# Kernel tuning notes

Measured on AMD Instinct MI355X. Metric: run time of the kernel, lower is better.

## Reference

```python
import jax, jax.numpy as jnp
import numpy as np

B, S, D, H = 2, 2048, 1024, 16
DH = D // H
EPS = 1e-12


def setup_inputs() -> dict:
    key = jax.random.key(0)
    ks = jax.random.split(key, 8)
    return {
        "query": jax.random.normal(ks[0], (B, S, D), jnp.float32),
        "key": jax.random.normal(ks[1], (B, S, D), jnp.float32),
        "value": jax.random.normal(ks[2], (B, S, D), jnp.float32),
        "mask": jax.random.randint(ks[3], (B, S), 0, 2, jnp.int32),
        "Wq": jax.random.normal(ks[4], (D, D), jnp.float32) * 0.02,
        "bq": jnp.zeros((D,), jnp.float32),
        "Wk": jax.random.normal(ks[5], (D, D), jnp.float32) * 0.02,
        "bk": jnp.zeros((D,), jnp.float32),
        "Wv": jax.random.normal(ks[6], (D, D), jnp.float32) * 0.02,
        "bv": jnp.zeros((D,), jnp.float32),
        "gamma": jnp.ones((D,), jnp.float32),
        "beta": jnp.zeros((D,), jnp.float32),
    }


def _split_heads(x):
    # [B,S,D] -> [B,H,S,DH]
    return x.reshape(B, S, H, DH).transpose(0, 2, 1, 3)


def reference(query, key, value, mask, Wq, bq, Wk, bk, Wv, bv, gamma, beta):
    q = _split_heads(query @ Wq + bq)
    k = _split_heads(key @ Wk + bk)
    v = _split_heads(value @ Wv + bv)

    scale = 1.0 / jnp.sqrt(jnp.float32(DH))
    scores = jnp.einsum("bhqd,bhkd->bhqk", q, k) * scale  # [B,H,S,S]
    maskf = mask.astype(jnp.float32)  # [B,S]
    scores = scores - 10000.0 * (1.0 - maskf[:, None, None, :])
    attn = jax.nn.softmax(scores, axis=-1)  # dropout disabled (eval mode)

    h = jnp.einsum("bhqk,bhkd->bhqd", attn, v)
    h = h.transpose(0, 2, 1, 3).reshape(B, S, D)

    x = query + h
    u = jnp.mean(x, axis=-1, keepdims=True)
    s = jnp.mean((x - u) ** 2, axis=-1, keepdims=True)
    xn = (x - u) / jnp.sqrt(s + EPS)
    return gamma * xn + beta
```

## Files before the change

kernel.cpp:

```cpp
#include <hip/hip_runtime.h>
#include <math.h>

#define B_  2
#define S_  2048
#define D_  1024
#define H_  16
#define DH_ 64
#define M_  (B_*S_)

typedef short v8s __attribute__((ext_vector_type(8)));
typedef float v4f __attribute__((ext_vector_type(4)));
typedef unsigned short u16;

__device__ __forceinline__ u16 f2bf(float f) {
    unsigned u = __float_as_uint(f);
    u = u + 0x7FFFu + ((u >> 16) & 1u);
    return (u16)(u >> 16);
}

__global__ __launch_bounds__(256)
void cvt_bf16_kernel(const float* __restrict__ X0, const float* __restrict__ X1,
                     const float* __restrict__ X2, u16* __restrict__ Y)
{
    const float* X = (blockIdx.y == 0) ? X0 : (blockIdx.y == 1) ? X1 : X2;
    u16* out = Y + (size_t)blockIdx.y * M_ * D_;
    const size_t i = ((size_t)blockIdx.x * 256 + threadIdx.x) * 8;
    float4 a = *(const float4*)&X[i];
    float4 b = *(const float4*)&X[i + 4];
    u16 tmp[8];
    tmp[0] = f2bf(a.x); tmp[1] = f2bf(a.y); tmp[2] = f2bf(a.z); tmp[3] = f2bf(a.w);
    tmp[4] = f2bf(b.x); tmp[5] = f2bf(b.y); tmp[6] = f2bf(b.z); tmp[7] = f2bf(b.w);
    *(v8s*)&out[i] = *(v8s*)&tmp[0];
}

__global__ __launch_bounds__(256)
void transpose_w_kernel(const float* __restrict__ W0, const float* __restrict__ W1,
                        const float* __restrict__ W2, u16* __restrict__ WtAll)
{
    __shared__ u16 TS[64][66];
    const float* W = (blockIdx.z == 0) ? W0 : (blockIdx.z == 1) ? W1 : W2;
    u16* out = WtAll + (size_t)blockIdx.z * D_ * D_;
    const int k0 = blockIdx.x * 64;
    const int n0 = blockIdx.y * 64;
    const int t = threadIdx.x;
    const int r = t >> 2, c = t & 3;

    #pragma unroll
    for (int u = 0; u < 4; ++u) {
        int nc = (c + 4 * u) * 4;
        float4 v = *(const float4*)&W[(size_t)(k0 + r) * D_ + n0 + nc];
        TS[r][nc + 0] = f2bf(v.x); TS[r][nc + 1] = f2bf(v.y);
        TS[r][nc + 2] = f2bf(v.z); TS[r][nc + 3] = f2bf(v.w);
    }
    __syncthreads();
    u16 tmp[16];
    #pragma unroll
    for (int u = 0; u < 16; ++u) tmp[u] = TS[c * 16 + u][r];
    u16* dst = &out[(size_t)(n0 + r) * D_ + k0 + c * 16];
    *(v8s*)&dst[0] = *(v8s*)&tmp[0];
    *(v8s*)&dst[8] = *(v8s*)&tmp[8];
}

__global__ __launch_bounds__(256)
void qkv_gemm_kernel(const u16* __restrict__ XbfAll, const u16* __restrict__ WtAll,
                     const float* __restrict__ bq, const float* __restrict__ bk2,
                     const float* __restrict__ bv2,
                     u16* __restrict__ Qh, u16* __restrict__ Kh, u16* __restrict__ Vh)
{
    __shared__ u16 SA[128 * 32];
    __shared__ u16 SB[128 * 32];

    const int z = blockIdx.z;
    const u16* X  = XbfAll + (size_t)z * M_ * D_;
    const u16* Wt = WtAll  + (size_t)z * D_ * D_;
    const float* bias = (z == 0) ? bq : (z == 1) ? bk2 : bv2;
    u16* Y = (z == 0) ? Qh : (z == 1) ? Kh : Vh;

    const int t = threadIdx.x;
    const int lane = t & 63;
    const int w = t >> 6;
    const int g = lane >> 4;
    const int l15 = lane & 15;
    const int wr = (w >> 1) * 64;
    const int wc = (w & 1) * 64;
    const int row0 = blockIdx.y * 128;
    const int col0 = blockIdx.x * 128;

    v4f acc[4][4];
    #pragma unroll
    for (int m = 0; m < 4; ++m)
        #pragma unroll
        for (int n = 0; n < 4; ++n)
            acc[m][n] = (v4f){0.f, 0.f, 0.f, 0.f};

    const int r0s = w * 32 + (lane >> 2);
    const int cphys = lane & 3;

    for (int k0 = 0; k0 < D_; k0 += 32) {
        __syncthreads();
        #pragma unroll
        for (int c = 0; c < 2; ++c) {
            const int r = r0s + c * 16;
            const int clog = cphys ^ ((r >> 1) & 3);
            const u16* asrc = &X [(size_t)(row0 + r) * D_ + k0 + clog * 8];
            const u16* bsrc = &Wt[(size_t)(col0 + r) * D_ + k0 + clog * 8];
            __builtin_amdgcn_global_load_lds(
                (const __attribute__((address_space(1))) void*)asrc,
                (__attribute__((address_space(3))) void*)&SA[(w * 32 + c * 16) * 32],
                16, 0, 0);
            __builtin_amdgcn_global_load_lds(
                (const __attribute__((address_space(1))) void*)bsrc,
                (__attribute__((address_space(3))) void*)&SB[(w * 32 + c * 16) * 32],
                16, 0, 0);
        }
        __syncthreads();

        v8s av[4], bvv[4];
        #pragma unroll
        for (int m = 0; m < 4; ++m) {
            const int r = wr + m * 16 + l15;
            av[m] = *(const v8s*)&SA[r * 32 + (g ^ ((r >> 1) & 3)) * 8];
        }
        #pragma unroll
        for (int n = 0; n < 4; ++n) {
            const int r = wc + n * 16 + l15;
            bvv[n] = *(const v8s*)&SB[r * 32 + (g ^ ((r >> 1) & 3)) * 8];
        }
        #pragma unroll
        for (int m = 0; m < 4; ++m)
            #pragma unroll
            for (int n = 0; n < 4; ++n)
                acc[m][n] = __builtin_amdgcn_mfma_f32_16x16x32_bf16(av[m], bvv[n], acc[m][n], 0, 0, 0);
    }

    #pragma unroll
    for (int n = 0; n < 4; ++n) {
        int col = col0 + wc + n * 16 + l15;
        float bb = bias[col];
        int h = col >> 6, d = col & 63;
        #pragma unroll
        for (int m = 0; m < 4; ++m) {
            #pragma unroll
            for (int i = 0; i < 4; ++i) {
                int row = row0 + wr + m * 16 + g * 4 + i;
                int b = row >> 11, s = row & (S_ - 1);
                Y[(((size_t)(b * H_ + h)) * S_ + s) * DH_ + d] = f2bf(acc[m][n][i] + bb);
            }
        }
    }
}

__global__ __launch_bounds__(256)
void transpose_v_kernel(const u16* __restrict__ Vh, u16* __restrict__ Vt)
{
    __shared__ u16 TS[64][66];
    const int bh = blockIdx.y;
    const int s0 = blockIdx.x * 64;
    const int t = threadIdx.x;
    const int r = t >> 2, c = t & 3;

    {
        const u16* src = Vh + ((size_t)(bh * S_ + s0 + r)) * DH_ + c * 16;
        v8s a = *(const v8s*)&src[0];
        v8s b = *(const v8s*)&src[8];
        *(v8s*)&TS[r][c * 16]     = a;
        *(v8s*)&TS[r][c * 16 + 8] = b;
    }
    __syncthreads();
    u16 tmp[16];
    #pragma unroll
    for (int u = 0; u < 16; ++u) tmp[u] = TS[c * 16 + u][r];
    u16* dst = Vt + ((size_t)(bh * DH_ + r)) * S_ + s0 + c * 16;
    *(v8s*)&dst[0] = *(v8s*)&tmp[0];
    *(v8s*)&dst[8] = *(v8s*)&tmp[8];
}

__global__ __launch_bounds__(256)
void attn_kernel(const u16* __restrict__ Qh, const u16* __restrict__ Kh,
                 const u16* __restrict__ Vt, const int* __restrict__ mask,
                 float* __restrict__ Hout)
{
    __shared__ u16 Ks[64][64];
    __shared__ u16 Vs[64][64];
    __shared__ u16 Ps[4][16][64];
    __shared__ float mb[64];

    const int t = threadIdx.x;
    const int lane = t & 63;
    const int w = t >> 6;
    const int g = lane >> 4;
    const int l15 = lane & 15;
    const int bh = blockIdx.y;
    const int b = bh >> 4;
    const int h = bh & 15;
    const int q0 = blockIdx.x * 64;

    const float SC = 0.18033688011112042f;
    const float MBIAS = -14426.950408889634f;

    v8s aq[2];
    {
        const u16* qb = Qh + ((size_t)bh * S_ + q0 + w * 16 + l15) * DH_;
        aq[0] = *(const v8s*)&qb[g * 8];
        aq[1] = *(const v8s*)&qb[32 + g * 8];
    }

    float lsum[4] = {0.f, 0.f, 0.f, 0.f};
    v4f Of[4];
    #pragma unroll
    for (int j = 0; j < 4; ++j) Of[j] = (v4f){0.f, 0.f, 0.f, 0.f};

    const int sk = t >> 3;
    const int sj = t & 7;
    const int swz_s = (sj ^ (sk & 7)) * 8;

    for (int kt = 0; kt < S_ / 64; ++kt) {
        const int kbase = kt * 64;
        const u16* ksrc0 = Kh + ((size_t)bh * S_ + kbase + sk) * DH_ + sj * 8;
        const u16* ksrc1 = Kh + ((size_t)bh * S_ + kbase + sk + 32) * DH_ + sj * 8;
        v8s kr0 = *(const v8s*)ksrc0;
        v8s kr1 = *(const v8s*)ksrc1;
        const u16* vsrc0 = Vt + ((size_t)bh * DH_ + sk) * S_ + kbase + sj * 8;
        const u16* vsrc1 = Vt + ((size_t)bh * DH_ + sk + 32) * S_ + kbase + sj * 8;
        v8s vr0 = *(const v8s*)vsrc0;
        v8s vr1 = *(const v8s*)vsrc1;
        int mv = 0;
        if (t < 64) mv = mask[b * S_ + kbase + t];

        __syncthreads();
        *(v8s*)&Ks[sk][swz_s]      = kr0;
        *(v8s*)&Ks[sk + 32][swz_s] = kr1;
        *(v8s*)&Vs[sk][swz_s]      = vr0;
        *(v8s*)&Vs[sk + 32][swz_s] = vr1;
        if (t < 64) mb[t] = mv ? 0.0f : MBIAS;
        __syncthreads();

        v4f sc4[4];
        #pragma unroll
        for (int j = 0; j < 4; ++j) sc4[j] = (v4f){0.f, 0.f, 0.f, 0.f};
        #pragma unroll
        for (int j = 0; j < 4; ++j) {
            const int kcol = j * 16 + l15;
            const int sx = kcol & 7;
            v8s bk0 = *(const v8s*)&Ks[kcol][((0 * 4 + g) ^ sx) * 8];
            v8s bk1 = *(const v8s*)&Ks[kcol][((1 * 4 + g) ^ sx) * 8];
            sc4[j] = __builtin_amdgcn_mfma_f32_16x16x32_bf16(aq[0], bk0, sc4[j], 0, 0, 0);
            sc4[j] = __builtin_amdgcn_mfma_f32_16x16x32_bf16(aq[1], bk1, sc4[j], 0, 0, 0);
        }
        float mbj[4];
        #pragma unroll
        for (int j = 0; j < 4; ++j) mbj[j] = mb[j * 16 + l15];

        #pragma unroll
        for (int i = 0; i < 4; ++i) {
            float p0 = __builtin_amdgcn_exp2f(fmaf(sc4[0][i], SC, mbj[0]));
            float p1 = __builtin_amdgcn_exp2f(fmaf(sc4[1][i], SC, mbj[1]));
            float p2 = __builtin_amdgcn_exp2f(fmaf(sc4[2][i], SC, mbj[2]));
            float p3 = __builtin_amdgcn_exp2f(fmaf(sc4[3][i], SC, mbj[3]));
            lsum[i] += (p0 + p1) + (p2 + p3);
            const int q = g * 4 + i;
            const int swz = 8 * (q & 7);
            Ps[w][q][(0 * 16 + l15) ^ swz] = f2bf(p0);
            Ps[w][q][(1 * 16 + l15) ^ swz] = f2bf(p1);
            Ps[w][q][(2 * 16 + l15) ^ swz] = f2bf(p2);
            Ps[w][q][(3 * 16 + l15) ^ swz] = f2bf(p3);
        }

        const int sq = l15 & 7;
        v8s pa0 = *(const v8s*)&Ps[w][l15][((0 + g) ^ sq) * 8];
        v8s pa1 = *(const v8s*)&Ps[w][l15][((4 + g) ^ sq) * 8];
        #pragma unroll
        for (int j = 0; j < 4; ++j) {
            const int dcol = j * 16 + l15;
            const int sx = dcol & 7;
            v8s bv0 = *(const v8s*)&Vs[dcol][((0 + g) ^ sx) * 8];
            v8s bv1 = *(const v8s*)&Vs[dcol][((4 + g) ^ sx) * 8];
            Of[j] = __builtin_amdgcn_mfma_f32_16x16x32_bf16(pa0, bv0, Of[j], 0, 0, 0);
            Of[j] = __builtin_amdgcn_mfma_f32_16x16x32_bf16(pa1, bv1, Of[j], 0, 0, 0);
        }
    }

    #pragma unroll
    for (int i = 0; i < 4; ++i) {
        lsum[i] += __shfl_xor(lsum[i], 1, 64);
        lsum[i] += __shfl_xor(lsum[i], 2, 64);
        lsum[i] += __shfl_xor(lsum[i], 4, 64);
        lsum[i] += __shfl_xor(lsum[i], 8, 64);
    }
    float inv[4];
    #pragma unroll
    for (int i = 0; i < 4; ++i) inv[i] = 1.0f / lsum[i];
    #pragma unroll
    for (int j = 0; j < 4; ++j) {
        #pragma unroll
        for (int i = 0; i < 4; ++i) {
            int q = q0 + w * 16 + g * 4 + i;
            Hout[((size_t)(b * S_ + q)) * D_ + h * DH_ + j * 16 + l15] = Of[j][i] * inv[i];
        }
    }
}

__global__ __launch_bounds__(256)
void ln_kernel(const float* __restrict__ query, const float* __restrict__ Hout,
               const float* __restrict__ gamma, const float* __restrict__ beta,
               float* __restrict__ out)
{
    __shared__ float ws1[4], ws2[4];
    const int row = blockIdx.x;
    const int tid = threadIdx.x;
    const size_t base = (size_t)row * D_ + tid * 4;

    float4 xq = *(const float4*)&query[base];
    float4 xh = *(const float4*)&Hout[base];
    float x[4] = { xq.x + xh.x, xq.y + xh.y, xq.z + xh.z, xq.w + xh.w };

    float sum = x[0] + x[1] + x[2] + x[3];
    float sq  = x[0]*x[0] + x[1]*x[1] + x[2]*x[2] + x[3]*x[3];
    #pragma unroll
    for (int off = 32; off >= 1; off >>= 1) {
        sum += __shfl_down(sum, off, 64);
        sq  += __shfl_down(sq,  off, 64);
    }
    if ((tid & 63) == 0) { ws1[tid >> 6] = sum; ws2[tid >> 6] = sq; }
    __syncthreads();
    sum = ws1[0] + ws1[1] + ws1[2] + ws1[3];
    sq  = ws2[0] + ws2[1] + ws2[2] + ws2[3];

    const float u    = sum * (1.0f / D_);
    const float var  = sq * (1.0f / D_) - u * u;
    const float rstd = rsqrtf(var + 1e-12f);

    float4 gv = *(const float4*)&gamma[tid * 4];
    float4 bv = *(const float4*)&beta[tid * 4];
    float4 o;
    o.x = gv.x * (x[0] - u) * rstd + bv.x;
    o.y = gv.y * (x[1] - u) * rstd + bv.y;
    o.z = gv.z * (x[2] - u) * rstd + bv.z;
    o.w = gv.w * (x[3] - u) * rstd + bv.w;
    *(float4*)&out[base] = o;
}

extern "C" void kernel_launch(void* const* d_in, const int* in_sizes, int n_in,
                              void* d_out, int out_size, void* d_ws, size_t ws_size,
                              hipStream_t stream)
{
    const float* query = (const float*)d_in[0];
    const float* key   = (const float*)d_in[1];
    const float* value = (const float*)d_in[2];
    const int*   mask  = (const int*)d_in[3];
    const float* Wq    = (const float*)d_in[4];
    const float* bq    = (const float*)d_in[5];
    const float* Wk    = (const float*)d_in[6];
    const float* bk    = (const float*)d_in[7];
    const float* Wv    = (const float*)d_in[8];
    const float* bv    = (const float*)d_in[9];
    const float* gamma = (const float*)d_in[10];
    const float* beta  = (const float*)d_in[11];
    float* out = (float*)d_out;

    char* ws = (char*)d_ws;
    u16* Xbf = (u16*)ws;                      ws += (size_t)3 * M_ * D_ * sizeof(u16);
    u16* Wt  = (u16*)ws;                      ws += (size_t)3 * D_ * D_ * sizeof(u16);
    u16* Qh  = (u16*)ws;                      ws += (size_t)M_ * D_ * sizeof(u16);
    u16* Kh  = (u16*)ws;                      ws += (size_t)M_ * D_ * sizeof(u16);
    u16* Vh  = (u16*)ws;                      ws += (size_t)M_ * D_ * sizeof(u16);
    u16* Vt  = (u16*)ws;                      ws += (size_t)M_ * D_ * sizeof(u16);
    float* Ho = (float*)ws;

    cvt_bf16_kernel<<<dim3(M_ * D_ / 2048, 3), 256, 0, stream>>>(query, key, value, Xbf);
    transpose_w_kernel<<<dim3(16, 16, 3), 256, 0, stream>>>(Wq, Wk, Wv, Wt);
    qkv_gemm_kernel<<<dim3(D_ / 128, M_ / 128, 3), 256, 0, stream>>>(
        Xbf, Wt, bq, bk, bv, Qh, Kh, Vh);
    transpose_v_kernel<<<dim3(S_ / 64, B_ * H_), 256, 0, stream>>>(Vh, Vt);
    attn_kernel<<<dim3(S_ / 64, B_ * H_), 256, 0, stream>>>(Qh, Kh, Vt, mask, Ho);
    ln_kernel<<<M_, 256, 0, stream>>>(query, Ho, gamma, beta, out);
}
```

Measured before the change: 238.3 us.

## Use 32x32 MFMA with BK=64 in QKV GEMM, fuse V transpose into epilogue

Rewrites the QKV projection GEMM to use 32x32x16 bf16 MFMA tiles with a 64-wide K step and an XOR-swizzled LDS layout, halving the number of K-loop barriers. The V output is written directly in transposed layout from the GEMM epilogue, which removes the separate transpose kernel and its round trip through memory. The attention P conversion switches from round-to-nearest to truncating bf16, saving a few ALU ops per element at a small accuracy cost. The transposed V stores are strided by sequence, so they may coalesce poorly.

```diff
diff --git a/kernel.cpp b/kernel.cpp
--- a/kernel.cpp
+++ b/kernel.cpp
@@ -8,14 +8,18 @@
 #define DH_ 64
 #define M_  (B_*S_)
 
-typedef short v8s __attribute__((ext_vector_type(8)));
-typedef float v4f __attribute__((ext_vector_type(4)));
+typedef short v8s  __attribute__((ext_vector_type(8)));
+typedef float v4f  __attribute__((ext_vector_type(4)));
+typedef float f32x16 __attribute__((ext_vector_type(16)));
 typedef unsigned short u16;
 
 __device__ __forceinline__ u16 f2bf(float f) {
     unsigned u = __float_as_uint(f);
     u = u + 0x7FFFu + ((u >> 16) & 1u);
     return (u16)(u >> 16);
+}
+__device__ __forceinline__ u16 f2bf_t(float f) {
+    return (u16)(__float_as_uint(f) >> 16);
 }
 
 __global__ __launch_bounds__(256)
@@ -65,114 +69,100 @@
 void qkv_gemm_kernel(const u16* __restrict__ XbfAll, const u16* __restrict__ WtAll,
                      const float* __restrict__ bq, const float* __restrict__ bk2,
                      const float* __restrict__ bv2,
-                     u16* __restrict__ Qh, u16* __restrict__ Kh, u16* __restrict__ Vh)
-{
-    __shared__ u16 SA[128 * 32];
-    __shared__ u16 SB[128 * 32];
+                     u16* __restrict__ Qh, u16* __restrict__ Kh, u16* __restrict__ Vt)
+{
+    __shared__ u16 SA[128 * 64];
+    __shared__ u16 SB[128 * 64];
 
     const int z = blockIdx.z;
     const u16* X  = XbfAll + (size_t)z * M_ * D_;
     const u16* Wt = WtAll  + (size_t)z * D_ * D_;
     const float* bias = (z == 0) ? bq : (z == 1) ? bk2 : bv2;
-    u16* Y = (z == 0) ? Qh : (z == 1) ? Kh : Vh;
 
     const int t = threadIdx.x;
     const int lane = t & 63;
     const int w = t >> 6;
-    const int g = lane >> 4;
-    const int l15 = lane & 15;
+    const int l31 = lane & 31;
+    const int half = lane >> 5;
     const int wr = (w >> 1) * 64;
     const int wc = (w & 1) * 64;
     const int row0 = blockIdx.y * 128;
     const int col0 = blockIdx.x * 128;
 
-    v4f acc[4][4];
-    #pragma unroll
-    for (int m = 0; m < 4; ++m)
-        #pragma unroll
-        for (int n = 0; n < 4; ++n)
-            acc[m][n] = (v4f){0.f, 0.f, 0.f, 0.f};
-
-    const int r0s = w * 32 + (lane >> 2);
-    const int cphys = lane & 3;
-
-    for (int k0 = 0; k0 < D_; k0 += 32) {
+    f32x16 acc[2][2];
+    #pragma unroll
+    for (int mb = 0; mb < 2; ++mb)
+        #pragma unroll
+        for (int nb = 0; nb < 2; ++nb)
+            acc[mb][nb] = (f32x16)(0.0f);
+
+    const int srow = t >> 3;
+    const int pch  = t & 7;
+
+    for (int k0 = 0; k0 < D_; k0 += 64) {
         __syncthreads();
         #pragma unroll
-        for (int c = 0; c < 2; ++c) {
-            const int r = r0s + c * 16;
-            const int clog = cphys ^ ((r >> 1) & 3);
-            const u16* asrc = &X [(size_t)(row0 + r) * D_ + k0 + clog * 8];
-            const u16* bsrc = &Wt[(size_t)(col0 + r) * D_ + k0 + clog * 8];
+        for (int c = 0; c < 4; ++c) {
+            const int r = c * 32 + srow;
+            const int lch = pch ^ (r & 7);
+            const u16* asrc = &X [(size_t)(row0 + r) * D_ + k0 + lch * 8];
+            const u16* bsrc = &Wt[(size_t)(col0 + r) * D_ + k0 + lch * 8];
             __builtin_amdgcn_global_load_lds(
                 (const __attribute__((address_space(1))) void*)asrc,
-                (__attribute__((address_space(3))) void*)&SA[(w * 32 + c * 16) * 32],
+                (__attribute__((address_space(3))) void*)&SA[r * 64 + pch * 8],
                 16, 0, 0);
             __builtin_amdgcn_global_load_lds(
                 (const __attribute__((address_space(1))) void*)bsrc,
-                (__attribute__((address_space(3))) void*)&SB[(w * 32 + c * 16) * 32],
+                (__attribute__((address_space(3))) void*)&SB[r * 64 + pch * 8],
                 16, 0, 0);
         }
         __syncthreads();
 
-        v8s av[4], bvv[4];
-        #pragma unroll
-        for (int m = 0; m < 4; ++m) {
-            const int r = wr + m * 16 + l15;
-            av[m] = *(const v8s*)&SA[r * 32 + (g ^ ((r >> 1) & 3)) * 8];
-        }
-        #pragma unroll
-        for (int n = 0; n < 4; ++n) {
-            const int r = wc + n * 16 + l15;
-            bvv[n] = *(const v8s*)&SB[r * 32 + (g ^ ((r >> 1) & 3)) * 8];
-        }
-        #pragma unroll
-        for (int m = 0; m < 4; ++m)
+        #pragma unroll
+        for (int ks = 0; ks < 4; ++ks) {
+            v8s av[2], bv[2];
             #pragma unroll
-            for (int n = 0; n < 4; ++n)
-                acc[m][n] = __builtin_amdgcn_mfma_f32_16x16x32_bf16(av[m], bvv[n], acc[m][n], 0, 0, 0);
-    }
-
-    #pragma unroll
-    for (int n = 0; n < 4; ++n) {
-        int col = col0 + wc + n * 16 + l15;
-        float bb = bias[col];
-        int h = col >> 6, d = col & 63;
-        #pragma unroll
-        for (int m = 0; m < 4; ++m) {
+            for (int mb = 0; mb < 2; ++mb) {
+                const int r = wr + mb * 32 + l31;
+                const int ch = (ks * 2 + half) ^ (r & 7);
+                av[mb] = *(const v8s*)&SA[r * 64 + ch * 8];
+            }
             #pragma unroll
-            for (int i = 0; i < 4; ++i) {
-                int row = row0 + wr + m * 16 + g * 4 + i;
-                int b = row >> 11, s = row & (S_ - 1);
-                Y[(((size_t)(b * H_ + h)) * S_ + s) * DH_ + d] = f2bf(acc[m][n][i] + bb);
+            for (int nb = 0; nb < 2; ++nb) {
+                const int r = wc + nb * 32 + l31;
+                const int ch = (ks * 2 + half) ^ (r & 7);
+                bv[nb] = *(const v8s*)&SB[r * 64 + ch * 8];
             }
-        }
-    }
-}
-
-__global__ __launch_bounds__(256)
-void transpose_v_kernel(const u16* __restrict__ Vh, u16* __restrict__ Vt)
-{
-    __shared__ u16 TS[64][66];
-    const int bh = blockIdx.y;
-    const int s0 = blockIdx.x * 64;
-    const int t = threadIdx.x;
-    const int r = t >> 2, c = t & 3;
-
-    {
-        const u16* src = Vh + ((size_t)(bh * S_ + s0 + r)) * DH_ + c * 16;
-        v8s a = *(const v8s*)&src[0];
-        v8s b = *(const v8s*)&src[8];
-        *(v8s*)&TS[r][c * 16]     = a;
-        *(v8s*)&TS[r][c * 16 + 8] = b;
-    }
-    __syncthreads();
-    u16 tmp[16];
-    #pragma unroll
-    for (int u = 0; u < 16; ++u) tmp[u] = TS[c * 16 + u][r];
-    u16* dst = Vt + ((size_t)(bh * DH_ + r)) * S_ + s0 + c * 16;
-    *(v8s*)&dst[0] = *(v8s*)&tmp[0];
-    *(v8s*)&dst[8] = *(v8s*)&tmp[8];
+            #pragma unroll
+            for (int mb = 0; mb < 2; ++mb)
+                #pragma unroll
+                for (int nb = 0; nb < 2; ++nb)
+                    acc[mb][nb] = __builtin_amdgcn_mfma_f32_32x32x16_bf16(
+                        av[mb], bv[nb], acc[mb][nb], 0, 0, 0);
+        }
+    }
+
+    #pragma unroll
+    for (int nb = 0; nb < 2; ++nb) {
+        const int col = col0 + wc + nb * 32 + l31;
+        const float bb = bias[col];
+        const int h = col >> 6, d = col & 63;
+        #pragma unroll
+        for (int mb = 0; mb < 2; ++mb) {
+            #pragma unroll
+            for (int rg = 0; rg < 16; ++rg) {
+                const int row = row0 + wr + mb * 32 + (rg & 3) + 8 * (rg >> 2) + 4 * half;
+                const int b = row >> 11, s = row & (S_ - 1);
+                const u16 o = f2bf(acc[mb][nb][rg] + bb);
+                if (z == 0)
+                    Qh[(((size_t)(b * H_ + h)) * S_ + s) * DH_ + d] = o;
+                else if (z == 1)
+                    Kh[(((size_t)(b * H_ + h)) * S_ + s) * DH_ + d] = o;
+                else
+                    Vt[(((size_t)(b * H_ + h)) * DH_ + d) * S_ + s] = o;
+            }
+        }
+    }
 }
 
 __global__ __launch_bounds__(256)
@@ -260,10 +250,10 @@
             lsum[i] += (p0 + p1) + (p2 + p3);
             const int q = g * 4 + i;
             const int swz = 8 * (q & 7);
-            Ps[w][q][(0 * 16 + l15) ^ swz] = f2bf(p0);
-            Ps[w][q][(1 * 16 + l15) ^ swz] = f2bf(p1);
-            Ps[w][q][(2 * 16 + l15) ^ swz] = f2bf(p2);
-            Ps[w][q][(3 * 16 + l15) ^ swz] = f2bf(p3);
+            Ps[w][q][(0 * 16 + l15) ^ swz] = f2bf_t(p0);
+            Ps[w][q][(1 * 16 + l15) ^ swz] = f2bf_t(p1);
+            Ps[w][q][(2 * 16 + l15) ^ swz] = f2bf_t(p2);
+            Ps[w][q][(3 * 16 + l15) ^ swz] = f2bf_t(p3);
         }
 
         const int sq = l15 & 7;
@@ -363,15 +353,13 @@
     u16* Wt  = (u16*)ws;                      ws += (size_t)3 * D_ * D_ * sizeof(u16);
     u16* Qh  = (u16*)ws;                      ws += (size_t)M_ * D_ * sizeof(u16);
     u16* Kh  = (u16*)ws;                      ws += (size_t)M_ * D_ * sizeof(u16);
-    u16* Vh  = (u16*)ws;                      ws += (size_t)M_ * D_ * sizeof(u16);
     u16* Vt  = (u16*)ws;                      ws += (size_t)M_ * D_ * sizeof(u16);
     float* Ho = (float*)ws;
 
     cvt_bf16_kernel<<<dim3(M_ * D_ / 2048, 3), 256, 0, stream>>>(query, key, value, Xbf);
     transpose_w_kernel<<<dim3(16, 16, 3), 256, 0, stream>>>(Wq, Wk, Wv, Wt);
     qkv_gemm_kernel<<<dim3(D_ / 128, M_ / 128, 3), 256, 0, stream>>>(
-        Xbf, Wt, bq, bk, bv, Qh, Kh, Vh);
-    transpose_v_kernel<<<dim3(S_ / 64, B_ * H_), 256, 0, stream>>>(Vh, Vt);
+        Xbf, Wt, bq, bk, bv, Qh, Kh, Vt);
     attn_kernel<<<dim3(S_ / 64, B_ * H_), 256, 0, stream>>>(Qh, Kh, Vt, mask, Ho);
     ln_kernel<<<M_, 256, 0, stream>>>(query, Ho, gamma, beta, out);
 }
```

After: 245.0 us. 1.03x slower.
